# Kernel tuning notes

Hardware: AMD Instinct MI355X
Metric: run time of the kernel (lower is better)

Reference implementation:

```python
import jax, jax.numpy as jnp
import numpy as np

WS = 7            # window size
HEADS = 4
DIM = 128         # hidden_dim
HEAD_DIM = 128    # wrapper passes head_dim=hidden_dim (faithful to source)
INNER = HEADS * HEAD_DIM   # 512
MLP = 4 * DIM
PATCH = 4
DISP = WS // 2
NEG = -1e9


def _ln(x, g, b, eps=1e-5):
    m = jnp.mean(x, -1, keepdims=True)
    v = jnp.mean((x - m) ** 2, -1, keepdims=True)
    return (x - m) * jax.lax.rsqrt(v + eps) * g + b


_coords = np.stack(np.meshgrid(np.arange(WS), np.arange(WS), indexing='ij'), -1).reshape(-1, 2)
REL_IDX = jnp.asarray(_coords[None] - _coords[:, None] + WS - 1)  # (ws^2, ws^2, 2)


def _build_masks():
    n = WS * WS
    ul = np.zeros((n, n), np.float32)
    ul[-DISP * WS:, : -DISP * WS] = NEG
    ul[: -DISP * WS, -DISP * WS:] = NEG
    lr = np.zeros((WS, WS, WS, WS), np.float32)
    lr[:, -DISP:, :, : -DISP] = NEG
    lr[:, : -DISP, :, -DISP:] = NEG
    return jnp.asarray(ul), jnp.asarray(lr.reshape(n, n))

UL_MASK, LR_MASK = _build_masks()


def _win_attn(x, w_qkv, pos, w_o, b_o, shifted):
    b, H, W, _ = x.shape
    if shifted:
        x = jnp.roll(x, (-DISP, -DISP), axis=(1, 2))
    nh, nw = H // WS, W // WS
    qkv = x @ w_qkv  # (b, H, W, 3*INNER)

    def to_win(t):  # -> (b, heads, n_windows, ws*ws, head_dim)
        t = t.reshape(b, nh, WS, nw, WS, HEADS, HEAD_DIM)
        return t.transpose(0, 5, 1, 3, 2, 4, 6).reshape(b, HEADS, nh * nw, WS * WS, HEAD_DIM)

    q, k, v = map(to_win, jnp.split(qkv, 3, axis=-1))
    dots = jnp.einsum('bhwid,bhwjd->bhwij', q, k) * (HEAD_DIM ** -0.5)
    dots = dots + pos[REL_IDX[..., 0], REL_IDX[..., 1]]  # shared across heads (berniwal)
    if shifted:
        dots = dots.at[:, :, -nw:].add(UL_MASK)
        dots = dots.at[:, :, nw - 1::nw].add(LR_MASK)
    attn = jax.nn.softmax(dots, axis=-1)
    out = jnp.einsum('bhwij,bhwjd->bhwid', attn, v)
    out = out.reshape(b, HEADS, nh, nw, WS, WS, HEAD_DIM).transpose(0, 2, 4, 3, 5, 1, 6)
    out = out.reshape(b, H, W, INNER) @ w_o + b_o
    if shifted:
        out = jnp.roll(out, (DISP, DISP), axis=(1, 2))
    return out


def _block(x, ga1, be1, w_qkv, pos, w_o, b_o, ga2, be2, w1, b1, w2, b2, shifted):
    x = x + _win_attn(_ln(x, ga1, be1), w_qkv, pos, w_o, b_o, shifted)
    h = jax.nn.gelu(_ln(x, ga2, be2) @ w1 + b1, approximate=False) @ w2 + b2
    return x + h


def _patch_embed(x, w, b):  # Unfold(patch) + Linear, channel-major feature order
    B, C, H, W = x.shape
    nh, nw = H // PATCH, W // PATCH
    x = x.reshape(B, C, nh, PATCH, nw, PATCH).transpose(0, 2, 4, 1, 3, 5)
    return x.reshape(B, nh, nw, C * PATCH * PATCH) @ w + b


def setup_inputs() -> dict:
    key = jax.random.key(0)
    ks = iter(jax.random.split(key, 48))

    def nrm(shape, s=0.02):
        return jax.random.normal(next(ks), shape, dtype=jnp.float32) * s

    inp = {'x': jax.random.normal(next(ks), (32, 3, 224, 224), dtype=jnp.float32)}
    inp['w_pe'] = nrm((3 * PATCH * PATCH, DIM))
    inp['b_pe'] = jnp.zeros((DIM,), jnp.float32)
    for s in ('a', 'b'):
        inp['ga1_' + s] = jnp.ones((DIM,), jnp.float32)
        inp['be1_' + s] = jnp.zeros((DIM,), jnp.float32)
        inp['w_qkv_' + s] = nrm((DIM, 3 * INNER))
        inp['pos_' + s] = nrm((2 * WS - 1, 2 * WS - 1), 1.0)
        inp['w_o_' + s] = nrm((INNER, DIM))
        inp['b_o_' + s] = jnp.zeros((DIM,), jnp.float32)
        inp['ga2_' + s] = jnp.ones((DIM,), jnp.float32)
        inp['be2_' + s] = jnp.zeros((DIM,), jnp.float32)
        inp['w_m1_' + s] = nrm((DIM, MLP))
        inp['b_m1_' + s] = jnp.zeros((MLP,), jnp.float32)
        inp['w_m2_' + s] = nrm((MLP, DIM))
        inp['b_m2_' + s] = jnp.zeros((DIM,), jnp.float32)
    return inp


def reference(x, w_pe, b_pe,
              ga1_a, be1_a, w_qkv_a, pos_a, w_o_a, b_o_a, ga2_a, be2_a, w_m1_a, b_m1_a, w_m2_a, b_m2_a,
              ga1_b, be1_b, w_qkv_b, pos_b, w_o_b, b_o_b, ga2_b, be2_b, w_m1_b, b_m1_b, w_m2_b, b_m2_b):
    h = _patch_embed(x, w_pe, b_pe)  # (B, 56, 56, DIM)
    h = _block(h, ga1_a, be1_a, w_qkv_a, pos_a, w_o_a, b_o_a, ga2_a, be2_a, w_m1_a, b_m1_a, w_m2_a, b_m2_a, False)
    h = _block(h, ga1_b, be1_b, w_qkv_b, pos_b, w_o_b, b_o_b, ga2_b, be2_b, w_m1_b, b_m1_b, w_m2_b, b_m2_b, True)
    return h
```

## Files before the change

### kernel.cpp

```cpp
#include <hip/hip_runtime.h>

typedef __attribute__((ext_vector_type(8))) short bf16x8;
typedef __attribute__((ext_vector_type(4))) short bf16x4;
typedef __attribute__((ext_vector_type(4))) float f32x4;
typedef __attribute__((ext_vector_type(2))) unsigned u32x2;

#define MFMA16(a, b, c) __builtin_amdgcn_mfma_f32_16x16x32_bf16(a, b, c, 0, 0, 0)

static __device__ __forceinline__ short f2bf(float f) {
    union { float f; unsigned u; } x; x.f = f;
    unsigned r = x.u + 0x7FFFu + ((x.u >> 16) & 1u);
    return (short)(r >> 16);
}

static __device__ __forceinline__ unsigned cvtpk(float lo, float hi) {
    unsigned r;
    asm("v_cvt_pk_bf16_f32 %0, %1, %2" : "=v"(r) : "v"(lo), "v"(hi));
    return r;
}

static __device__ __forceinline__ void gload16(const void* g, void* l) {
    __builtin_amdgcn_global_load_lds((const __attribute__((address_space(1))) void*)g,
                                     (__attribute__((address_space(3))) void*)l, 16, 0, 0);
}

__global__ void convT_kernel(const float* __restrict__ in, short* __restrict__ out, int K, int N) {
    int idx = blockIdx.x * 256 + threadIdx.x;
    if (idx < K * N) {
        int k = idx % K, n = idx / K;
        out[idx] = f2bf(in[(size_t)k * N + n]);
    }
}

__global__ void tabgen_kernel(const float* __restrict__ pos_a, const float* __restrict__ pos_b,
                              float* __restrict__ tab) {
    int v = blockIdx.x;
    const float* pos = (v == 0) ? pos_a : pos_b;
    for (int e = threadIdx.x; e < 4096; e += 256) {
        int row = e >> 6, key = e & 63;
        float val;
        if (key >= 49) val = -1e9f;
        else if (row >= 49) val = 0.f;
        else {
            int qi = row / 7, qj = row - qi * 7, ki = key / 7, kj = key - ki * 7;
            val = pos[(ki - qi + 6) * 13 + (kj - qj + 6)];
            if (v >= 1) {
                bool wh7 = (v - 1) & 2, ww7 = (v - 1) & 1;
                if (wh7 && ((qi >= 4) != (ki >= 4))) val += -1e9f;
                if (ww7 && ((qj >= 4) != (kj >= 4))) val += -1e9f;
            }
        }
        tab[v * 4096 + e] = val;
    }
}

__global__ __launch_bounds__(256) void patchln_kernel(const float* __restrict__ x,
                                                      const float* __restrict__ w,
                                                      const float* __restrict__ bias,
                                                      const float* __restrict__ g,
                                                      const float* __restrict__ bta,
                                                      float* __restrict__ out,
                                                      short* __restrict__ xn) {
    __shared__ float s_in[2][48];
    __shared__ float red[2][2][2];
    const int tid = threadIdx.x;
    const int half = tid >> 7, c = tid & 127;
    const int winh = (tid >> 6) & 1, lane = tid & 63;
    const int t = blockIdx.x * 2 + half;
    const int b = t / 3136, rem = t - b * 3136;
    const int hp = rem / 56, wp = rem - hp * 56;
    if (c < 48) {
        int cin = c >> 4, py = (c >> 2) & 3, px = c & 3;
        s_in[half][c] = x[((size_t)(b * 3 + cin) * 224 + hp * 4 + py) * 224 + wp * 4 + px];
    }
    __syncthreads();
    float acc = bias[c];
#pragma unroll
    for (int k = 0; k < 48; ++k) acc += s_in[half][k] * w[k * 128 + c];
    out[(size_t)t * 128 + c] = acc;
    float s1 = acc, s2 = acc * acc;
#pragma unroll
    for (int o = 32; o > 0; o >>= 1) { s1 += __shfl_xor(s1, o); s2 += __shfl_xor(s2, o); }
    if (lane == 0) { red[half][winh][0] = s1; red[half][winh][1] = s2; }
    __syncthreads();
    s1 = red[half][0][0] + red[half][1][0];
    s2 = red[half][0][1] + red[half][1][1];
    float mean = s1 * (1.f / 128.f);
    float var = s2 * (1.f / 128.f) - mean * mean;
    float rstd = rsqrtf(var + 1e-5f);
    xn[(size_t)t * 128 + c] = f2bf((acc - mean) * rstd * g[c] + bta[c]);
}

template <int SHIFTED>
__global__ __launch_bounds__(256, 3) void attn_kernel(const short* __restrict__ xn,
                                                      const short* __restrict__ wqkvT,
                                                      const float* __restrict__ tab,
                                                      const short* __restrict__ zpad,
                                                      short* __restrict__ aout) {
    __shared__ short smem[24576];
    short* s_x = smem;
    short* s_q = smem + 8192;
    short* s_k = smem + 16384;

    const int tid = threadIdx.x;
    const int wid = tid >> 6, lane = tid & 63;
    const int l15 = lane & 15, l4 = lane >> 4, klo = l4 * 8;
    const int bid = blockIdx.x;
    const int win = bid & 63, head = (bid >> 6) & 3, b = bid >> 8;
    const int wh = win >> 3, ww = win & 7;

    int trow[4];
#pragma unroll
    for (int j = 0; j < 4; ++j) {
        int r = j * 16 + l15; r = (r > 48) ? 48 : r;
        int wi = (r * 37) >> 8, wj = r - wi * 7;
        int hh = wh * 7 + wi, wp = ww * 7 + wj;
        if (SHIFTED) { hh += 3; if (hh >= 56) hh -= 56; wp += 3; if (wp >= 56) wp -= 56; }
        trow[j] = (b * 56 + hh) * 56 + wp;
    }

#pragma unroll
    for (int it = 0; it < 4; ++it) {
        int slot = it * 256 + tid;
        int row = slot >> 4, scol = slot & 15;
        int colb = (scol * 16) ^ ((row & 7) << 4);
        const char* g;
        if (row < 49) {
            int wi = (row * 37) >> 8, wj = row - wi * 7;
            int hh = wh * 7 + wi, wp = ww * 7 + wj;
            if (SHIFTED) { hh += 3; if (hh >= 56) hh -= 56; wp += 3; if (wp >= 56) wp -= 56; }
            int t = (b * 56 + hh) * 56 + wp;
            g = (const char*)(xn + (size_t)t * 128) + colb;
        } else {
            g = (const char*)zpad + colb;
        }
        gload16(g, (char*)smem + (it * 256 + wid * 64) * 16);
    }
    __syncthreads();

    const f32x4 zero4 = {0.f, 0.f, 0.f, 0.f};

    {
        const short* Wq = wqkvT + (size_t)(head * 128) * 128;
        const short* Wk = wqkvT + (size_t)(512 + head * 128) * 128;
        f32x4 aq[2][4], ak[2][4];
#pragma unroll
        for (int mw = 0; mw < 2; ++mw)
#pragma unroll
            for (int j = 0; j < 4; ++j) { aq[mw][j] = zero4; ak[mw][j] = zero4; }
#pragma unroll
        for (int k0 = 0; k0 < 4; ++k0) {
            bf16x8 bx[4], awq[2], awk[2];
#pragma unroll
            for (int j = 0; j < 4; ++j) {
                int row = j * 16 + l15;
                bx[j] = *(const bf16x8*)((const char*)s_x + row * 256 + ((k0 * 64 + l4 * 16) ^ ((row & 7) << 4)));
            }
#pragma unroll
            for (int mw = 0; mw < 2; ++mw) {
                awq[mw] = *(const bf16x8*)(Wq + (size_t)(wid * 32 + mw * 16 + l15) * 128 + k0 * 32 + klo);
                awk[mw] = *(const bf16x8*)(Wk + (size_t)(wid * 32 + mw * 16 + l15) * 128 + k0 * 32 + klo);
            }
            __builtin_amdgcn_s_setprio(1);
#pragma unroll
            for (int mw = 0; mw < 2; ++mw)
#pragma unroll
                for (int j = 0; j < 4; ++j) {
                    aq[mw][j] = MFMA16(awq[mw], bx[j], aq[mw][j]);
                    ak[mw][j] = MFMA16(awk[mw], bx[j], ak[mw][j]);
                }
            __builtin_amdgcn_s_setprio(0);
        }
#pragma unroll
        for (int mw = 0; mw < 2; ++mw)
#pragma unroll
            for (int j = 0; j < 4; ++j) {
                u32x2 pq = { cvtpk(aq[mw][j][0], aq[mw][j][1]), cvtpk(aq[mw][j][2], aq[mw][j][3]) };
                u32x2 pk = { cvtpk(ak[mw][j][0], ak[mw][j][1]), cvtpk(ak[mw][j][2], ak[mw][j][3]) };
                int row = j * 16 + l15;
                int colb = (wid * 64 + mw * 32 + l4 * 8) ^ ((row & 7) << 4);
                *(u32x2*)((char*)s_q + row * 256 + colb) = pq;
                *(u32x2*)((char*)s_k + row * 256 + colb) = pk;
            }
    }

    f32x4 av[4][2];
#pragma unroll
    for (int m = 0; m < 4; ++m)
#pragma unroll
        for (int n = 0; n < 2; ++n) av[m][n] = zero4;
    {
        const short* Wv = wqkvT + (size_t)(1024 + head * 128) * 128;
#pragma unroll
        for (int k0 = 0; k0 < 4; ++k0) {
            bf16x8 ax[4], bw[2];
#pragma unroll
            for (int m = 0; m < 4; ++m) {
                int row = m * 16 + l15;
                ax[m] = *(const bf16x8*)((const char*)s_x + row * 256 + ((k0 * 64 + l4 * 16) ^ ((row & 7) << 4)));
            }
#pragma unroll
            for (int n = 0; n < 2; ++n)
                bw[n] = *(const bf16x8*)(Wv + (size_t)(wid * 32 + n * 16 + l15) * 128 + k0 * 32 + klo);
            __builtin_amdgcn_s_setprio(1);
#pragma unroll
            for (int m = 0; m < 4; ++m)
#pragma unroll
                for (int n = 0; n < 2; ++n) av[m][n] = MFMA16(ax[m], bw[n], av[m][n]);
            __builtin_amdgcn_s_setprio(0);
        }
    }
    __syncthreads();

#pragma unroll
    for (int m = 0; m < 4; ++m)
#pragma unroll
        for (int n = 0; n < 2; ++n) {
            u32x2 pv = { cvtpk(av[m][n][0], av[m][n][1]), cvtpk(av[m][n][2], av[m][n][3]) };
            int hd = wid * 32 + n * 16 + l15;
            *(u32x2*)((char*)s_x + hd * 128 + ((m * 32 + l4 * 8) ^ ((hd & 7) << 4))) = pv;
        }

    const int qrow = wid * 16 + l15;
    f32x4 dt[4];
#pragma unroll
    for (int m = 0; m < 4; ++m) dt[m] = zero4;
#pragma unroll
    for (int k0 = 0; k0 < 4; ++k0) {
        bf16x8 bq = *(const bf16x8*)((const char*)s_q + qrow * 256 + ((k0 * 64 + l4 * 16) ^ ((qrow & 7) << 4)));
        __builtin_amdgcn_s_setprio(1);
#pragma unroll
        for (int m = 0; m < 4; ++m) {
            int krow = m * 16 + l15;
            bf16x8 akf = *(const bf16x8*)((const char*)s_k + krow * 256 + ((k0 * 64 + l4 * 16) ^ ((krow & 7) << 4)));
            dt[m] = MFMA16(akf, bq, dt[m]);
        }
        __builtin_amdgcn_s_setprio(0);
    }

    const int variant = SHIFTED ? (1 + ((wh == 7) ? 2 : 0) + ((ww == 7) ? 1 : 0)) : 0;
    const float* tv = tab + variant * 4096 + qrow * 64;
    const float SC = 0.08838834764831845f;
    float p[4][4];
    float mx = -3.0e38f;
#pragma unroll
    for (int m = 0; m < 4; ++m) {
        f32x4 tb = *(const f32x4*)(tv + m * 16 + l4 * 4);
#pragma unroll
        for (int r = 0; r < 4; ++r) {
            float d = dt[m][r] * SC + tb[r];
            p[m][r] = d;
            mx = fmaxf(mx, d);
        }
    }
    mx = fmaxf(mx, __shfl_xor(mx, 16));
    mx = fmaxf(mx, __shfl_xor(mx, 32));
    float sum = 0.f;
#pragma unroll
    for (int m = 0; m < 4; ++m)
#pragma unroll
        for (int r = 0; r < 4; ++r) { p[m][r] = __expf(p[m][r] - mx); sum += p[m][r]; }
    sum += __shfl_xor(sum, 16);
    sum += __shfl_xor(sum, 32);
    float inv = 1.f / sum;
#pragma unroll
    for (int m = 0; m < 4; ++m) {
        u32x2 pv = { cvtpk(p[m][0] * inv, p[m][1] * inv), cvtpk(p[m][2] * inv, p[m][3] * inv) };
        *(u32x2*)((char*)s_q + qrow * 256 + ((m * 32 + l4 * 8) ^ ((qrow & 7) << 4))) = pv;
    }
    __syncthreads();

    f32x4 o[2][4];
#pragma unroll
    for (int fn = 0; fn < 2; ++fn)
#pragma unroll
        for (int tm = 0; tm < 4; ++tm) o[fn][tm] = zero4;
#pragma unroll
    for (int k0 = 0; k0 < 2; ++k0) {
        bf16x8 ap[4], bv2[2];
#pragma unroll
        for (int tm = 0; tm < 4; ++tm) {
            int row = tm * 16 + l15;
            ap[tm] = *(const bf16x8*)((const char*)s_q + row * 256 + ((k0 * 64 + l4 * 16) ^ ((row & 7) << 4)));
        }
#pragma unroll
        for (int fn = 0; fn < 2; ++fn) {
            int hd = wid * 32 + fn * 16 + l15;
            bv2[fn] = *(const bf16x8*)((const char*)s_x + hd * 128 + ((k0 * 64 + l4 * 16) ^ ((hd & 7) << 4)));
        }
        __builtin_amdgcn_s_setprio(1);
#pragma unroll
        for (int fn = 0; fn < 2; ++fn)
#pragma unroll
            for (int tm = 0; tm < 4; ++tm) o[fn][tm] = MFMA16(bv2[fn], ap[tm], o[fn][tm]);
        __builtin_amdgcn_s_setprio(0);
    }
#pragma unroll
    for (int tm = 0; tm < 4; ++tm) {
        if (tm * 16 + l15 < 49) {
            short* dst = aout + (size_t)trow[tm] * 512 + head * 128 + wid * 32 + l4 * 4;
#pragma unroll
            for (int fn = 0; fn < 2; ++fn) {
                u32x2 pv = { cvtpk(o[fn][tm][0], o[fn][tm][1]), cvtpk(o[fn][tm][2], o[fn][tm][3]) };
                *(u32x2*)(dst + fn * 16) = pv;
            }
        }
    }
}

template <int K, int MODE>
__global__ __launch_bounds__(256, 2) void gemm2_kernel(const short* __restrict__ A,
                                                       const short* __restrict__ BT,
                                                       const float* __restrict__ bias,
                                                       const float* __restrict__ resid,
                                                       const float* __restrict__ g,
                                                       const float* __restrict__ bta,
                                                       float* __restrict__ outf,
                                                       short* __restrict__ outb,
                                                       int Ntot) {
    __shared__ char smem[32768];
    short* s_a = (short*)smem;
    short* s_b = (short*)(smem + 16384);
    float* red = (float*)smem;

    const int tid = threadIdx.x, wid = tid >> 6, lane = tid & 63;
    const int wr = wid >> 1, wc = wid & 1;
    const int l15 = lane & 15, l4 = lane >> 4;
    const int m0 = blockIdx.x * 128;
    const int nb0 = blockIdx.y * 128;

    const f32x4 zero4 = {0.f, 0.f, 0.f, 0.f};
    f32x4 acc[4][4];
#pragma unroll
    for (int m = 0; m < 4; ++m)
#pragma unroll
        for (int n = 0; n < 4; ++n) acc[m][n] = zero4;

    for (int kc = 0; kc < K / 64; ++kc) {
#pragma unroll
        for (int it = 0; it < 4; ++it) {
            int slot = it * 256 + tid;
            int row = slot >> 3, scol = slot & 7;
            int colb = (scol * 16) ^ ((row & 7) << 4);
            gload16((const char*)(A + (size_t)(m0 + row) * K + kc * 64) + colb,
                    (char*)smem + (it * 256 + wid * 64) * 16);
        }
#pragma unroll
        for (int it = 0; it < 4; ++it) {
            int slot = it * 256 + tid;
            int row = slot >> 3, scol = slot & 7;
            int colb = (scol * 16) ^ ((row & 7) << 4);
            gload16((const char*)(BT + (size_t)(nb0 + row) * K + kc * 64) + colb,
                    (char*)smem + 16384 + (it * 256 + wid * 64) * 16);
        }
        __syncthreads();
#pragma unroll
        for (int ks = 0; ks < 2; ++ks) {
            bf16x8 a[4], bfr[4];
#pragma unroll
            for (int m = 0; m < 4; ++m) {
                int row = wr * 64 + m * 16 + l15;
                a[m] = *(const bf16x8*)((const char*)s_a + row * 128 + ((ks * 64 + l4 * 16) ^ ((row & 7) << 4)));
            }
#pragma unroll
            for (int n = 0; n < 4; ++n) {
                int row = wc * 64 + n * 16 + l15;
                bfr[n] = *(const bf16x8*)((const char*)s_b + row * 128 + ((ks * 64 + l4 * 16) ^ ((row & 7) << 4)));
            }
            __builtin_amdgcn_s_setprio(1);
#pragma unroll
            for (int m = 0; m < 4; ++m)
#pragma unroll
                for (int n = 0; n < 4; ++n) acc[m][n] = MFMA16(a[m], bfr[n], acc[m][n]);
            __builtin_amdgcn_s_setprio(0);
        }
        __syncthreads();
    }

    float bv[4];
#pragma unroll
    for (int n = 0; n < 4; ++n) bv[n] = bias[nb0 + wc * 64 + n * 16 + l15];

    if (MODE == 0) {
#pragma unroll
        for (int m = 0; m < 4; ++m)
#pragma unroll
            for (int r = 0; r < 4; ++r) {
                int row = m0 + wr * 64 + m * 16 + l4 * 4 + r;
#pragma unroll
                for (int n = 0; n < 4; ++n) {
                    int col = nb0 + wc * 64 + n * 16 + l15;
                    float v = acc[m][n][r] + bv[n];
                    v = 0.5f * v * (1.f + erff(v * 0.70710678118f));
                    outb[(size_t)row * Ntot + col] = f2bf(v);
                }
            }
        return;
    }

    float s1[4][4], s2[4][4];
#pragma unroll
    for (int m = 0; m < 4; ++m)
#pragma unroll
        for (int r = 0; r < 4; ++r) {
            int row = m0 + wr * 64 + m * 16 + l4 * 4 + r;
            float a1 = 0.f, a2 = 0.f;
#pragma unroll
            for (int n = 0; n < 4; ++n) {
                int col = wc * 64 + n * 16 + l15;
                float v = acc[m][n][r] + bv[n] + resid[(size_t)row * 128 + col];
                acc[m][n][r] = v;
                a1 += v; a2 += v * v;
            }
            s1[m][r] = a1; s2[m][r] = a2;
        }

    if (MODE == 1) {
#pragma unroll
        for (int m = 0; m < 4; ++m)
#pragma unroll
            for (int r = 0; r < 4; ++r) {
#pragma unroll
                for (int o = 1; o < 16; o <<= 1) {
                    s1[m][r] += __shfl_xor(s1[m][r], o);
                    s2[m][r] += __shfl_xor(s2[m][r], o);
                }
            }
        __syncthreads();
#pragma unroll
        for (int m = 0; m < 4; ++m)
#pragma unroll
            for (int r = 0; r < 4; ++r) {
                if (l15 == m * 4 + r) {
                    int lrow = wr * 64 + m * 16 + l4 * 4 + r;
                    red[lrow * 4 + wc * 2] = s1[m][r];
                    red[lrow * 4 + wc * 2 + 1] = s2[m][r];
                }
            }
        __syncthreads();
    }

#pragma unroll
    for (int m = 0; m < 4; ++m)
#pragma unroll
        for (int r = 0; r < 4; ++r) {
            int lrow = wr * 64 + m * 16 + l4 * 4 + r;
            int row = m0 + lrow;
            float mean = 0.f, rstd = 0.f;
            if (MODE == 1) {
                float t1 = red[lrow * 4] + red[lrow * 4 + 2];
                float t2 = red[lrow * 4 + 1] + red[lrow * 4 + 3];
                mean = t1 * (1.f / 128.f);
                float var = t2 * (1.f / 128.f) - mean * mean;
                rstd = rsqrtf(var + 1e-5f);
            }
#pragma unroll
            for (int n = 0; n < 4; ++n) {
                int col = wc * 64 + n * 16 + l15;
                float v = acc[m][n][r];
                outf[(size_t)row * 128 + col] = v;
                if (MODE == 1)
                    outb[(size_t)row * 128 + col] = f2bf((v - mean) * rstd * g[col] + bta[col]);
            }
        }
}

extern "C" void kernel_launch(void* const* d_in, const int* in_sizes, int n_in,
                              void* d_out, int out_size, void* d_ws, size_t ws_size,
                              hipStream_t stream) {
    const float* x = (const float*)d_in[0];
    const float* w_pe = (const float*)d_in[1];
    const float* b_pe = (const float*)d_in[2];
    const float* P[24];
    for (int i = 0; i < 24; ++i) P[i] = (const float*)d_in[3 + i];

    float* out = (float*)d_out;
    const size_t TOK = 100352;

    short* xn = (short*)d_ws;
    short* abuf = xn + TOK * 128;
    short* wqkv = abuf + TOK * 512;
    short* wo = wqkv + 196608;
    short* wm1 = wo + 65536;
    short* wm2 = wm1 + 65536;
    float* tab = (float*)(wm2 + 65536);
    short* zpad = (short*)(tab + 5 * 4096);

    hipMemsetAsync(zpad, 0, 256, stream);
    tabgen_kernel<<<5, 256, 0, stream>>>(P[3], P[15], tab);

    patchln_kernel<<<50176, 256, 0, stream>>>(x, w_pe, b_pe, P[0], P[1], out, xn);

    for (int s = 0; s < 2; ++s) {
        convT_kernel<<<768, 256, 0, stream>>>(P[s * 12 + 2], wqkv, 128, 1536);
        convT_kernel<<<256, 256, 0, stream>>>(P[s * 12 + 4], wo, 512, 128);
        convT_kernel<<<256, 256, 0, stream>>>(P[s * 12 + 8], wm1, 128, 512);
        convT_kernel<<<256, 256, 0, stream>>>(P[s * 12 + 10], wm2, 512, 128);

        if (s == 0)
            attn_kernel<0><<<8192, 256, 0, stream>>>(xn, wqkv, tab, zpad, abuf);
        else
            attn_kernel<1><<<8192, 256, 0, stream>>>(xn, wqkv, tab, zpad, abuf);

        gemm2_kernel<512, 1><<<dim3(784, 1), 256, 0, stream>>>(
            abuf, wo, P[s * 12 + 5], out, P[s * 12 + 6], P[s * 12 + 7], out, xn, 128);

        gemm2_kernel<128, 0><<<dim3(784, 4), 256, 0, stream>>>(
            xn, wm1, P[s * 12 + 9], nullptr, nullptr, nullptr, nullptr, abuf, 512);

        if (s == 0)
            gemm2_kernel<512, 1><<<dim3(784, 1), 256, 0, stream>>>(
                abuf, wm2, P[11], out, P[12], P[13], out, xn, 128);
        else
            gemm2_kernel<512, 2><<<dim3(784, 1), 256, 0, stream>>>(
                abuf, wm2, P[23], out, nullptr, nullptr, out, nullptr, 128);
    }
}
```

Measured before the change: 640.0 us.

## Fuse MLP up-projection, GELU and down-projection into one kernel

Replaces the separate W1+GELU GEMM and W2 GEMM with a single mlp_kernel. Each block keeps its 128-token tile of normalized input in LDS, computes the 512-wide hidden in 128-column chunks with GELU applied in registers, and writes each chunk to LDS as bf16. The down-projection then accumulates from LDS, so the hidden activation never round-trips through global memory. In exchange the kernel uses 64KB of LDS, which may lower occupancy, and it reads both weight matrices directly from global memory without staging them in LDS.

```diff
diff --git a/kernel.cpp b/kernel.cpp
--- a/kernel.cpp
+++ b/kernel.cpp
@@ -316,8 +316,7 @@
                                                        const float* __restrict__ g,
                                                        const float* __restrict__ bta,
                                                        float* __restrict__ outf,
-                                                       short* __restrict__ outb,
-                                                       int Ntot) {
+                                                       short* __restrict__ outb) {
     __shared__ char smem[32768];
     short* s_a = (short*)smem;
     short* s_b = (short*)(smem + 16384);
@@ -327,7 +326,6 @@
     const int wr = wid >> 1, wc = wid & 1;
     const int l15 = lane & 15, l4 = lane >> 4;
     const int m0 = blockIdx.x * 128;
-    const int nb0 = blockIdx.y * 128;
 
     const f32x4 zero4 = {0.f, 0.f, 0.f, 0.f};
     f32x4 acc[4][4];
@@ -350,7 +348,7 @@
             int slot = it * 256 + tid;
             int row = slot >> 3, scol = slot & 7;
             int colb = (scol * 16) ^ ((row & 7) << 4);
-            gload16((const char*)(BT + (size_t)(nb0 + row) * K + kc * 64) + colb,
+            gload16((const char*)(BT + (size_t)row * K + kc * 64) + colb,
                     (char*)smem + 16384 + (it * 256 + wid * 64) * 16);
         }
         __syncthreads();
@@ -379,24 +377,7 @@
 
     float bv[4];
 #pragma unroll
-    for (int n = 0; n < 4; ++n) bv[n] = bias[nb0 + wc * 64 + n * 16 + l15];
-
-    if (MODE == 0) {
-#pragma unroll
-        for (int m = 0; m < 4; ++m)
-#pragma unroll
-            for (int r = 0; r < 4; ++r) {
-                int row = m0 + wr * 64 + m * 16 + l4 * 4 + r;
-#pragma unroll
-                for (int n = 0; n < 4; ++n) {
-                    int col = nb0 + wc * 64 + n * 16 + l15;
-                    float v = acc[m][n][r] + bv[n];
-                    v = 0.5f * v * (1.f + erff(v * 0.70710678118f));
-                    outb[(size_t)row * Ntot + col] = f2bf(v);
-                }
-            }
-        return;
-    }
+    for (int n = 0; n < 4; ++n) bv[n] = bias[wc * 64 + n * 16 + l15];
 
     float s1[4][4], s2[4][4];
 #pragma unroll
@@ -465,6 +446,178 @@
         }
 }
 
+template <int MODE>
+__global__ __launch_bounds__(256, 2) void mlp_kernel(const short* __restrict__ xn_in,
+                                                     const short* __restrict__ wm1T,
+                                                     const short* __restrict__ wm2T,
+                                                     const float* __restrict__ b1,
+                                                     const float* __restrict__ b2,
+                                                     const float* __restrict__ resid,
+                                                     const float* __restrict__ g,
+                                                     const float* __restrict__ bta,
+                                                     float* __restrict__ outf,
+                                                     short* __restrict__ outb) {
+    __shared__ char smem[65536];
+    short* s_x = (short*)smem;
+    short* s_h = (short*)(smem + 32768);
+    float* red = (float*)smem;
+
+    const int tid = threadIdx.x, wid = tid >> 6, lane = tid & 63;
+    const int wr = wid >> 1, wc = wid & 1;
+    const int l15 = lane & 15, l4 = lane >> 4, klo = l4 * 8;
+    const int m0 = blockIdx.x * 128;
+
+#pragma unroll
+    for (int it = 0; it < 8; ++it) {
+        int slot = it * 256 + tid;
+        int row = slot >> 4, scol = slot & 15;
+        int colb = (scol * 16) ^ ((row & 7) << 4);
+        gload16((const char*)(xn_in + (size_t)(m0 + row) * 128) + colb,
+                (char*)smem + (it * 256 + wid * 64) * 16);
+    }
+    __syncthreads();
+
+    const f32x4 zero4 = {0.f, 0.f, 0.f, 0.f};
+    f32x4 acc[4][4];
+#pragma unroll
+    for (int m = 0; m < 4; ++m)
+#pragma unroll
+        for (int n = 0; n < 4; ++n) acc[m][n] = zero4;
+
+#pragma unroll
+    for (int hc = 0; hc < 4; ++hc) {
+        f32x4 ah[2][8];
+#pragma unroll
+        for (int mw = 0; mw < 2; ++mw)
+#pragma unroll
+            for (int j = 0; j < 8; ++j) ah[mw][j] = zero4;
+#pragma unroll
+        for (int ks = 0; ks < 4; ++ks) {
+            bf16x8 bx[8], aw[2];
+#pragma unroll
+            for (int j = 0; j < 8; ++j) {
+                int row = j * 16 + l15;
+                bx[j] = *(const bf16x8*)((const char*)s_x + row * 256 + ((ks * 64 + l4 * 16) ^ ((row & 7) << 4)));
+            }
+#pragma unroll
+            for (int mw = 0; mw < 2; ++mw)
+                aw[mw] = *(const bf16x8*)(wm1T + (size_t)(hc * 128 + wid * 32 + mw * 16 + l15) * 128 + ks * 32 + klo);
+            __builtin_amdgcn_s_setprio(1);
+#pragma unroll
+            for (int mw = 0; mw < 2; ++mw)
+#pragma unroll
+                for (int j = 0; j < 8; ++j) ah[mw][j] = MFMA16(aw[mw], bx[j], ah[mw][j]);
+            __builtin_amdgcn_s_setprio(0);
+        }
+#pragma unroll
+        for (int mw = 0; mw < 2; ++mw) {
+            f32x4 b4 = *(const f32x4*)(b1 + hc * 128 + wid * 32 + mw * 16 + l4 * 4);
+#pragma unroll
+            for (int j = 0; j < 8; ++j) {
+                float v[4];
+#pragma unroll
+                for (int r = 0; r < 4; ++r) {
+                    float t = ah[mw][j][r] + b4[r];
+                    v[r] = 0.5f * t * (1.f + erff(t * 0.70710678118f));
+                }
+                u32x2 pv = { cvtpk(v[0], v[1]), cvtpk(v[2], v[3]) };
+                int tok = j * 16 + l15;
+                *(u32x2*)((char*)s_h + tok * 256 + ((wid * 64 + mw * 32 + l4 * 8) ^ ((tok & 7) << 4))) = pv;
+            }
+        }
+        __syncthreads();
+#pragma unroll
+        for (int ks = 0; ks < 4; ++ks) {
+            bf16x8 a[4], bfr[4];
+#pragma unroll
+            for (int m = 0; m < 4; ++m) {
+                int row = wr * 64 + m * 16 + l15;
+                a[m] = *(const bf16x8*)((const char*)s_h + row * 256 + ((ks * 64 + l4 * 16) ^ ((row & 7) << 4)));
+            }
+#pragma unroll
+            for (int n = 0; n < 4; ++n)
+                bfr[n] = *(const bf16x8*)(wm2T + (size_t)(wc * 64 + n * 16 + l15) * 512 + hc * 128 + ks * 32 + klo);
+            __builtin_amdgcn_s_setprio(1);
+#pragma unroll
+            for (int m = 0; m < 4; ++m)
+#pragma unroll
+                for (int n = 0; n < 4; ++n) acc[m][n] = MFMA16(a[m], bfr[n], acc[m][n]);
+            __builtin_amdgcn_s_setprio(0);
+        }
+        __syncthreads();
+    }
+
+    float bv[4];
+#pragma unroll
+    for (int n = 0; n < 4; ++n) bv[n] = b2[wc * 64 + n * 16 + l15];
+
+    float s1[4][4], s2[4][4];
+#pragma unroll
+    for (int m = 0; m < 4; ++m)
+#pragma unroll
+        for (int r = 0; r < 4; ++r) {
+            int row = m0 + wr * 64 + m * 16 + l4 * 4 + r;
+            float a1 = 0.f, a2 = 0.f;
+#pragma unroll
+            for (int n = 0; n < 4; ++n) {
+                int col = wc * 64 + n * 16 + l15;
+                float v = acc[m][n][r] + bv[n] + resid[(size_t)row * 128 + col];
+                acc[m][n][r] = v;
+                a1 += v; a2 += v * v;
+            }
+            s1[m][r] = a1; s2[m][r] = a2;
+        }
+
+    if (MODE == 1) {
+#pragma unroll
+        for (int m = 0; m < 4; ++m)
+#pragma unroll
+            for (int r = 0; r < 4; ++r) {
+#pragma unroll
+                for (int o = 1; o < 16; o <<= 1) {
+                    s1[m][r] += __shfl_xor(s1[m][r], o);
+                    s2[m][r] += __shfl_xor(s2[m][r], o);
+                }
+            }
+        __syncthreads();
+#pragma unroll
+        for (int m = 0; m < 4; ++m)
+#pragma unroll
+            for (int r = 0; r < 4; ++r) {
+                if (l15 == m * 4 + r) {
+                    int lrow = wr * 64 + m * 16 + l4 * 4 + r;
+                    red[lrow * 4 + wc * 2] = s1[m][r];
+                    red[lrow * 4 + wc * 2 + 1] = s2[m][r];
+                }
+            }
+        __syncthreads();
+    }
+
+#pragma unroll
+    for (int m = 0; m < 4; ++m)
+#pragma unroll
+        for (int r = 0; r < 4; ++r) {
+            int lrow = wr * 64 + m * 16 + l4 * 4 + r;
+            int row = m0 + lrow;
+            float mean = 0.f, rstd = 0.f;
+            if (MODE == 1) {
+                float t1 = red[lrow * 4] + red[lrow * 4 + 2];
+                float t2 = red[lrow * 4 + 1] + red[lrow * 4 + 3];
+                mean = t1 * (1.f / 128.f);
+                float var = t2 * (1.f / 128.f) - mean * mean;
+                rstd = rsqrtf(var + 1e-5f);
+            }
+#pragma unroll
+            for (int n = 0; n < 4; ++n) {
+                int col = wc * 64 + n * 16 + l15;
+                float v = acc[m][n][r];
+                outf[(size_t)row * 128 + col] = v;
+                if (MODE == 1)
+                    outb[(size_t)row * 128 + col] = f2bf((v - mean) * rstd * g[col] + bta[col]);
+            }
+        }
+}
+
 extern "C" void kernel_launch(void* const* d_in, const int* in_sizes, int n_in,
                               void* d_out, int out_size, void* d_ws, size_t ws_size,
                               hipStream_t stream) {
@@ -502,17 +655,14 @@
         else
             attn_kernel<1><<<8192, 256, 0, stream>>>(xn, wqkv, tab, zpad, abuf);
 
-        gemm2_kernel<512, 1><<<dim3(784, 1), 256, 0, stream>>>(
-            abuf, wo, P[s * 12 + 5], out, P[s * 12 + 6], P[s * 12 + 7], out, xn, 128);
-
-        gemm2_kernel<128, 0><<<dim3(784, 4), 256, 0, stream>>>(
-            xn, wm1, P[s * 12 + 9], nullptr, nullptr, nullptr, nullptr, abuf, 512);
+        gemm2_kernel<512, 1><<<784, 256, 0, stream>>>(
+            abuf, wo, P[s * 12 + 5], out, P[s * 12 + 6], P[s * 12 + 7], out, xn);
 
         if (s == 0)
-            gemm2_kernel<512, 1><<<dim3(784, 1), 256, 0, stream>>>(
-                abuf, wm2, P[11], out, P[12], P[13], out, xn, 128);
+            mlp_kernel<1><<<784, 256, 0, stream>>>(
+                xn, wm1, wm2, P[9], P[11], out, P[12], P[13], out, xn);
         else
-            gemm2_kernel<512, 2><<<dim3(784, 1), 256, 0, stream>>>(
-                abuf, wm2, P[23], out, nullptr, nullptr, out, nullptr, 128);
-    }
-}
+            mlp_kernel<2><<<784, 256, 0, stream>>>(
+                xn, wm1, wm2, P[21], P[23], out, nullptr, nullptr, out, nullptr);
+    }
+}
```

Measured after the change: 673.8 us. 5.3% more time.
